# Performance work log

Measured on AMD Instinct MI355X. Metric: run time of the kernel, lower is better.

## Reference

```python
import jax, jax.numpy as jnp
import numpy as np
from jax import lax

E = 20          # num experts / classes
BN_EPS = 1e-5


def _conv(x, w, b=None):
    # NCHW conv, stride 1, 'same' padding (kernel 3x3 or 1x1)
    y = lax.conv_general_dilated(x, w, (1, 1), 'SAME',
                                 dimension_numbers=('NCHW', 'OIHW', 'NCHW'))
    return y if b is None else y + b[None, :, None, None]


def _lrelu(x):
    return jnp.where(x >= 0, x, 0.2 * x)


def _bn(x, g, b, m, v):
    # inference-mode batchnorm
    scale = g * lax.rsqrt(v + BN_EPS)
    return x * scale[None, :, None, None] + (b - m * scale)[None, :, None, None]


def setup_inputs() -> dict:
    key = jax.random.key(0)
    ks = iter(jax.random.split(key, 40))
    def w(shape):
        return jax.random.normal(next(ks), shape, jnp.float32) * 0.05
    d = {}
    d['x'] = jax.random.normal(next(ks), (2, 3, 192, 192), jnp.float32)
    d['noise'] = jax.random.normal(next(ks), (2, 128, 192, 192), jnp.float32)
    # classification head
    d['cls_w1'] = w((64, 3, 3, 3));    d['cls_b1'] = jnp.zeros((64,), jnp.float32)
    d['cls_w2'] = w((128, 64, 3, 3));  d['cls_b2'] = jnp.zeros((128,), jnp.float32)
    d['cls_w3'] = w((256, 128, 3, 3)); d['cls_b3'] = jnp.zeros((256,), jnp.float32)
    d['cls_w4'] = w((512, 256, 1, 1)); d['cls_b4'] = jnp.zeros((512,), jnp.float32)
    d['cls_w5'] = w((E, 512, 1, 1));   d['cls_b5'] = jnp.zeros((E,), jnp.float32)
    for c, i in ((128, 1), (256, 2), (512, 3)):
        d[f'bn{i}_g'] = jnp.ones((c,), jnp.float32)
        d[f'bn{i}_b'] = jnp.zeros((c,), jnp.float32)
        d[f'bn{i}_m'] = jnp.zeros((c,), jnp.float32)
        d[f'bn{i}_v'] = jnp.ones((c,), jnp.float32)
    # 20 expert encoders (stacked on leading axis)
    d['enc_w1'] = w((E, 32, 3, 3, 3));    d['enc_b1'] = jnp.zeros((E, 32), jnp.float32)
    d['enc_w2'] = w((E, 64, 32, 3, 3));   d['enc_b2'] = jnp.zeros((E, 64), jnp.float32)
    d['enc_w3'] = w((E, 128, 64, 3, 3));  d['enc_b3'] = jnp.zeros((E, 128), jnp.float32)
    d['enc_w4'] = w((E, 128, 128, 3, 3)); d['enc_b4'] = jnp.zeros((E, 128), jnp.float32)
    # decoder (legacy=False: first two 1x1 convs have no bias)
    d['dec_w1'] = w((64, 128, 1, 1))
    d['dec_w2'] = w((32, 64, 1, 1))
    d['dec_w3'] = w((3, 32, 1, 1)); d['dec_b3'] = jnp.zeros((3,), jnp.float32)
    return d


def reference(x, noise,
              cls_w1, cls_b1, cls_w2, cls_b2, cls_w3, cls_b3,
              cls_w4, cls_b4, cls_w5, cls_b5,
              bn1_g, bn1_b, bn1_m, bn1_v,
              bn2_g, bn2_b, bn2_m, bn2_v,
              bn3_g, bn3_b, bn3_m, bn3_v,
              enc_w1, enc_b1, enc_w2, enc_b2, enc_w3, enc_b3, enc_w4, enc_b4,
              dec_w1, dec_w2, dec_w3, dec_b3):
    B, _, H, W = x.shape
    C = enc_w4.shape[1]  # 128
    # --- classification / routing ---
    h = _lrelu(_conv(x, cls_w1, cls_b1))
    h = _lrelu(_bn(_conv(h, cls_w2, cls_b2), bn1_g, bn1_b, bn1_m, bn1_v))
    h = _lrelu(_bn(_conv(h, cls_w3, cls_b3), bn2_g, bn2_b, bn2_m, bn2_v))
    h = _lrelu(_bn(_conv(h, cls_w4, cls_b4), bn3_g, bn3_b, bn3_m, bn3_v))
    classes = jax.nn.softmax(_conv(h, cls_w5, cls_b5), axis=1)  # [B,E,H,W]
    idx = jnp.argmax(classes, axis=1)  # [B,H,W] top-1 expert per pixel

    # --- run all 20 dense encoders (faithful to original torch.where masking) ---
    def enc(w1, b1, w2, b2, w3, b3, w4, b4):
        e = _lrelu(_conv(x, w1, b1))
        e = _lrelu(_conv(e, w2, b2))
        e = _lrelu(_conv(e, w3, b3))
        return _conv(e, w4, b4)
    embs = jax.vmap(enc)(enc_w1, enc_b1, enc_w2, enc_b2,
                         enc_w3, enc_b3, enc_w4, enc_b4)  # [E,B,128,H,W]
    embs = jnp.moveaxis(embs, 0, 1)  # [B,E,128,H,W]
    sel_idx = jnp.broadcast_to(idx[:, None, None, :, :], (B, 1, C, H, W))
    emb = jnp.take_along_axis(embs, sel_idx, axis=1)[:, 0]  # [B,128,H,W]

    # --- decode with additive noise ---
    d = _conv(emb + noise, dec_w1)
    d = _conv(d, dec_w2)
    out = _conv(d, dec_w3, dec_b3)  # [B,3,H,W]

    # --- load balancing loss ---
    one_hot = jax.nn.one_hot(idx, E, dtype=jnp.float32)          # [B,H,W,E]
    density = one_hot.reshape(B, -1, E).mean(axis=1)             # [B,E]
    density_proxy = classes.reshape(B, E, -1).mean(axis=-1)      # [B,E]
    lb = (density_proxy * density).mean() * float(E * E)
    return out, lb * 0.1
```

## Files before the change

kernel.cpp:

```cpp
#include <hip/hip_runtime.h>
#include <hip/hip_bf16.h>

typedef __hip_bfloat16 bf16;
typedef unsigned short u16;
typedef short s16x8 __attribute__((ext_vector_type(8)));
typedef float f32x4 __attribute__((ext_vector_type(4)));
#define MFMA16(a, b, c) __builtin_amdgcn_mfma_f32_16x16x32_bf16(a, b, c, 0, 0, 0)

#define HW_   36864
#define WP_   194
#define HWP_  37636
#define W_    192
#define SP_   9216

__device__ __forceinline__ float ldin(const void* p, size_t i, int f32) {
    return f32 ? ((const float*)p)[i] : __bfloat162float(((const bf16*)p)[i]);
}
__device__ __forceinline__ int probe_f32(const void* pr) {
    return ((const unsigned*)pr)[0] == 0x3F800000u;
}
__device__ __forceinline__ u16 f2bf(float f) {
    bf16 h = __float2bfloat16(f);
    return *reinterpret_cast<u16*>(&h);
}

__global__ __launch_bounds__(256) void pad_x_k(const void* __restrict__ x,
                                               float* __restrict__ xpad,
                                               const void* __restrict__ pr) {
    const int f32 = probe_f32(pr);
    int i = blockIdx.x * 256 + threadIdx.x;
    if (i >= 2 * 3 * HW_) return;
    int w = i % W_;
    int h = (i / W_) % W_;
    int c = i / HW_;
    xpad[(size_t)c * HWP_ + (size_t)(h + 1) * WP_ + (w + 1)] = ldin(x, i, f32);
}

__global__ __launch_bounds__(256) void conv3x3_k(
    const float* __restrict__ in, const void* __restrict__ wgt,
    const void* __restrict__ bias, const void* __restrict__ bng,
    const void* __restrict__ bnb, const void* __restrict__ bnm,
    const void* __restrict__ bnv, float* __restrict__ out,
    int Cin, int Cout, int lrelu, const void* __restrict__ pr)
{
    extern __shared__ float wl[];
    const int f32 = probe_f32(pr);
    const int tid = threadIdx.x;
    const int co0 = blockIdx.y * 8;
    const int b   = blockIdx.z;
    const int n = Cin * 72;
    for (int i = tid; i < n; i += 256) {
        int u = i & 7, r = i >> 3;
        int ci = r / 9, tap = r - ci * 9;
        wl[i] = ldin(wgt, ((size_t)(co0 + u) * Cin + ci) * 9 + tap, f32);
    }
    __syncthreads();

    const int pixb = blockIdx.x * 1024 + tid;
    int off[4];
#pragma unroll
    for (int p = 0; p < 4; ++p) {
        int pix = pixb + p * 256;
        int h = pix / W_, w = pix - h * W_;
        off[p] = (h + 1) * WP_ + (w + 1);
    }
    float acc[32];
#pragma unroll
    for (int i = 0; i < 32; ++i) acc[i] = 0.f;

    const int doff[9] = {-(WP_+1), -WP_, -(WP_-1), -1, 0, 1, WP_-1, WP_, WP_+1};
    const float* inb = in + (size_t)b * Cin * HWP_;
    for (int ci = 0; ci < Cin; ++ci) {
        const float* ip = inb + (size_t)ci * HWP_;
        const float* wp = wl + ci * 72;
#pragma unroll
        for (int tap = 0; tap < 9; ++tap) {
            const float4 wa = *(const float4*)(wp + tap * 8);
            const float4 wb = *(const float4*)(wp + tap * 8 + 4);
            const int d = doff[tap];
            float v[4];
#pragma unroll
            for (int p = 0; p < 4; ++p) v[p] = ip[off[p] + d];
#pragma unroll
            for (int p = 0; p < 4; ++p) {
                acc[p*8+0] += v[p] * wa.x;  acc[p*8+1] += v[p] * wa.y;
                acc[p*8+2] += v[p] * wa.z;  acc[p*8+3] += v[p] * wa.w;
                acc[p*8+4] += v[p] * wb.x;  acc[p*8+5] += v[p] * wb.y;
                acc[p*8+6] += v[p] * wb.z;  acc[p*8+7] += v[p] * wb.w;
            }
        }
    }

#pragma unroll
    for (int u = 0; u < 8; ++u) {
        const int co = co0 + u;
        float s = 1.f, t = 0.f;
        if (bng) {
            float g = ldin(bng, co, f32), bb = ldin(bnb, co, f32);
            float m = ldin(bnm, co, f32), vv = ldin(bnv, co, f32);
            s = g * rsqrtf(vv + 1e-5f);
            t = bb - m * s;
        }
        const float bs = bias ? ldin(bias, co, f32) : 0.f;
        float* op = out + ((size_t)b * Cout + co) * HWP_;
#pragma unroll
        for (int p = 0; p < 4; ++p) {
            float val = (acc[p*8+u] + bs) * s + t;
            if (lrelu) val = val >= 0.f ? val : 0.2f * val;
            op[off[p]] = val;
        }
    }
}

__global__ __launch_bounds__(256) void conv1x1s_k(
    const float* __restrict__ in, const void* __restrict__ wgt,
    const void* __restrict__ bias, const void* __restrict__ bng,
    const void* __restrict__ bnb, const void* __restrict__ bnm,
    const void* __restrict__ bnv, float* __restrict__ out,
    int Cin, int pix0, const void* __restrict__ pr)
{
    extern __shared__ float wl[];
    const int f32 = probe_f32(pr);
    const int tid = threadIdx.x;
    const int co0 = blockIdx.y * 8;
    const int b   = blockIdx.z;
    const int n = Cin * 8;
    for (int i = tid; i < n; i += 256) {
        int u = i & 7, ci = i >> 3;
        wl[i] = ldin(wgt, (size_t)(co0 + u) * Cin + ci, f32);
    }
    __syncthreads();

    const int pixb = pix0 + blockIdx.x * 1024 + tid;
    int off[4], lp[4];
#pragma unroll
    for (int p = 0; p < 4; ++p) {
        int pix = pixb + p * 256;
        lp[p] = pix - pix0;
        int h = pix / W_, w = pix - h * W_;
        off[p] = (h + 1) * WP_ + (w + 1);
    }
    float acc[32];
#pragma unroll
    for (int i = 0; i < 32; ++i) acc[i] = 0.f;

    for (int ci = 0; ci < Cin; ++ci) {
        const float* ip = in + ((size_t)b * Cin + ci) * HWP_;
        const float4 wa = *(const float4*)(wl + ci * 8);
        const float4 wb = *(const float4*)(wl + ci * 8 + 4);
        float v[4];
#pragma unroll
        for (int p = 0; p < 4; ++p) v[p] = ip[off[p]];
#pragma unroll
        for (int p = 0; p < 4; ++p) {
            acc[p*8+0] += v[p] * wa.x;  acc[p*8+1] += v[p] * wa.y;
            acc[p*8+2] += v[p] * wa.z;  acc[p*8+3] += v[p] * wa.w;
            acc[p*8+4] += v[p] * wb.x;  acc[p*8+5] += v[p] * wb.y;
            acc[p*8+6] += v[p] * wb.z;  acc[p*8+7] += v[p] * wb.w;
        }
    }

#pragma unroll
    for (int u = 0; u < 8; ++u) {
        const int co = co0 + u;
        float g = ldin(bng, co, f32), bb = ldin(bnb, co, f32);
        float m = ldin(bnm, co, f32), vv = ldin(bnv, co, f32);
        float s = g * rsqrtf(vv + 1e-5f);
        float t = bb - m * s;
        const float bs = ldin(bias, co, f32);
        float* op = out + ((size_t)b * 512 + co) * SP_;
#pragma unroll
        for (int p = 0; p < 4; ++p) {
            float val = (acc[p*8+u] + bs) * s + t;
            val = val >= 0.f ? val : 0.2f * val;
            op[lp[p]] = val;
        }
    }
}

__global__ __launch_bounds__(256) void heads_k(
    const float* __restrict__ c4q, const void* __restrict__ w5,
    const void* __restrict__ b5, int* __restrict__ idx,
    float* __restrict__ proxy, float* __restrict__ cntg, int pix0,
    const void* __restrict__ pr)
{
    extern __shared__ float wl[];
    __shared__ float sums[20];
    __shared__ float cnts[20];
    const int f32 = probe_f32(pr);
    const int tid = threadIdx.x;
    const int b = blockIdx.y;
    for (int i = tid; i < 512 * 20; i += 256) {
        int e = i % 20, ci = i / 20;
        wl[ci * 20 + e] = ldin(w5, (size_t)e * 512 + ci, f32);
    }
    if (tid < 20) { sums[tid] = 0.f; cnts[tid] = 0.f; }
    __syncthreads();

    const int lpix = blockIdx.x * 256 + tid;

    float acc[20];
#pragma unroll
    for (int e = 0; e < 20; ++e) acc[e] = ldin(b5, e, f32);
    const float* ip = c4q + (size_t)b * 512 * SP_;
    for (int ci = 0; ci < 512; ++ci) {
        const float v = ip[(size_t)ci * SP_ + lpix];
        const float* wp = wl + ci * 20;
#pragma unroll
        for (int e = 0; e < 20; ++e) acc[e] += v * wp[e];
    }

    float m = acc[0]; int am = 0;
#pragma unroll
    for (int e = 1; e < 20; ++e) if (acc[e] > m) { m = acc[e]; am = e; }
    float prb[20], ssum = 0.f;
#pragma unroll
    for (int e = 0; e < 20; ++e) { prb[e] = expf(acc[e] - m); ssum += prb[e]; }
    const float inv = 1.f / ssum;
    idx[b * HW_ + pix0 + lpix] = am;

    const int lane = tid & 63;
#pragma unroll
    for (int e = 0; e < 20; ++e) {
        float p = prb[e] * inv;
        p += __shfl_down(p, 32); p += __shfl_down(p, 16); p += __shfl_down(p, 8);
        p += __shfl_down(p, 4);  p += __shfl_down(p, 2);  p += __shfl_down(p, 1);
        if (lane == 0) atomicAdd(&sums[e], p);
        unsigned long long bal = __ballot(am == e);
        if (lane == 0) atomicAdd(&cnts[e], (float)__popcll(bal));
    }
    __syncthreads();
    if (tid < 20) {
        atomicAdd(&proxy[b * 20 + tid], sums[tid]);
        atomicAdd(&cntg[b * 20 + tid], cnts[tid]);
    }
}

__global__ __launch_bounds__(256) void wtx_k(const void* __restrict__ w,
                                             u16* __restrict__ wt,
                                             int Cout, int Cin, int nTot,
                                             const void* __restrict__ pr) {
    const int f32 = probe_f32(pr);
    int i = blockIdx.x * 256 + threadIdx.x;
    if (i >= nTot) return;
    int ci = i % Cin; int r = i / Cin;
    int co = r % Cout; r /= Cout;
    int tap = r % 9; int e = r / 9;
    size_t src = ((size_t)(e * Cout + co) * Cin + ci) * 9 + tap;
    wt[i] = f2bf(ldin(w, src, f32));
}

__global__ __launch_bounds__(512) void fused_expert_k(
    const float* __restrict__ xpad, const int* __restrict__ idx,
    const void* __restrict__ ew1, const void* __restrict__ eb1,
    const u16* __restrict__ Wt2, const void* __restrict__ eb2,
    const u16* __restrict__ Wt3, const void* __restrict__ eb3,
    const u16* __restrict__ Wt4, const void* __restrict__ eb4,
    float* __restrict__ emb, const void* __restrict__ pr)
{
    __shared__ __align__(16) char smem_[137216];
    u16*   e2s = (u16*)smem_;
    u16*   e3s = (u16*)(smem_ + 54272);
    u16*   e1s = (u16*)(smem_ + 54272);
    float* xs  = (float*)smem_;
    float* wl1 = (float*)(smem_ + 6912);
    u16*   w2s = (u16*)(smem_ + 86016);
    __shared__ int s_sel[256];
    __shared__ int s_wc[8];
    __shared__ unsigned long long s_selq[4];
    __shared__ u16 s_l3[324];
    __shared__ int s_c3;

    const int f32 = probe_f32(pr);
    const int tid  = threadIdx.x;
    const int lane = tid & 63, wv = tid >> 6;
    const int ml = lane & 15, q8 = (lane >> 4) * 8, m0 = (lane >> 4) * 4;
    const int b = blockIdx.y;
    const int eid = blockIdx.z;
    const int ty = blockIdx.x / 12, tx = blockIdx.x - ty * 12;
    const int Oh = ty * 16, Ow = tx * 16;

    {
        int sel = 0;
        if (tid < 256) {
            const int r = tid >> 4, c = tid & 15;
            sel = (idx[b * HW_ + (Oh + r) * W_ + (Ow + c)] == eid);
        }
        const unsigned long long m = __ballot(sel);
        if (lane == 0) {
            s_wc[wv] = __popcll(m);
            if (wv < 4) s_selq[wv] = m;
        }
        __syncthreads();
        int cnt = 0;
#pragma unroll
        for (int w = 0; w < 8; ++w) cnt += s_wc[w];
        if (cnt == 0) return;
        int pre = 0;
        for (int w = 0; w < wv; ++w) pre += s_wc[w];
        if (sel)
            s_sel[pre + __popcll(m & ((1ull << lane) - 1ull))] = tid;
    }

    if (wv == 0) {
        unsigned need = 0;
        const int r3 = lane;
        if (r3 < 18) {
            unsigned m = 0;
#pragma unroll
            for (int d = 0; d < 3; ++d) {
                const int r = r3 - 2 + d;
                if (r >= 0 && r < 16)
                    m |= (unsigned)((s_selq[r >> 2] >> ((r & 3) * 16)) & 0xFFFFull);
            }
            need = (m | (m << 1) | (m << 2)) & 0x3FFFFu;
        }
        const int pc = __popc(need);
        int inc = pc;
#pragma unroll
        for (int o = 1; o < 32; o <<= 1) {
            const int t = __shfl_up(inc, o);
            if (lane >= o) inc += t;
        }
        int k = inc - pc;
        unsigned mm = need;
        while (mm) {
            const int c = __ffs(mm) - 1;
            mm &= mm - 1;
            s_l3[k++] = (u16)(r3 * 18 + c);
        }
        if (lane == 17) s_c3 = inc;
    }

    for (int i = tid; i < 24 * 24 * 3; i += 512) {
        int ch = i % 3, pxl = i / 3;
        int r = pxl / 24, c = pxl - r * 24;
        int ir = Oh - 4 + r, ic = Ow - 4 + c;
        float v = 0.f;
        if (ir >= -1 && ir < 193 && ic >= -1 && ic < 193)
            v = xpad[((size_t)b * 3 + ch) * HWP_ + (size_t)(ir + 1) * WP_ + (ic + 1)];
        xs[pxl * 3 + ch] = v;
    }
    for (int i = tid; i < 896; i += 512) {
        if (i < 864) {
            int co = i & 31, k = i >> 5;
            int ci = k / 9, tap = k - ci * 9;
            wl1[i] = ldin(ew1, (size_t)eid * 864 + ((size_t)co * 3 + ci) * 9 + tap, f32);
        } else {
            wl1[i] = ldin(eb1, (size_t)eid * 32 + (i - 864), f32);
        }
    }
    {
        const u16* Wt2e = Wt2 + (size_t)eid * 9 * 64 * 32;
        for (int i = tid; i < 2304; i += 512) {
            int r = i >> 2, part = i & 3;
            *(uint4*)(w2s + (size_t)r * 40 + part * 8) =
                *(const uint4*)(Wt2e + (size_t)r * 32 + part * 8);
        }
    }
    __syncthreads();

    if (tid < 484) {
        const int p = tid;
        const int r1 = p / 22, c1 = p - r1 * 22;
        const int ir = Oh - 3 + r1, ic = Ow - 3 + c1;
        const int inimg = (ir >= 0 && ir < 192 && ic >= 0 && ic < 192);
        float a1[32];
#pragma unroll
        for (int co = 0; co < 32; ++co) a1[co] = 0.f;
        if (inimg) {
#pragma unroll
            for (int ci = 0; ci < 3; ++ci)
#pragma unroll
                for (int tap = 0; tap < 9; ++tap) {
                    const int dy = tap / 3, dx = tap - dy * 3;
                    const float xv = xs[((r1 + dy) * 24 + (c1 + dx)) * 3 + ci];
                    const float* wp = wl1 + (ci * 9 + tap) * 32;
#pragma unroll
                    for (int co = 0; co < 32; ++co) a1[co] += xv * wp[co];
                }
        }
        u16 pk[32];
#pragma unroll
        for (int co = 0; co < 32; ++co) {
            float v = 0.f;
            if (inimg) {
                v = a1[co] + wl1[864 + co];
                v = v >= 0.f ? v : 0.2f * v;
            }
            pk[co] = f2bf(v);
        }
#pragma unroll
        for (int ch = 0; ch < 4; ++ch)
            *(uint4*)(e1s + ((size_t)ch * 488 + p) * 8) = ((const uint4*)pk)[ch];
    }
    __syncthreads();

    {
        int pxv[4], r2v[4], c2v[4];
#pragma unroll
        for (int j = 0; j < 4; ++j) {
            int t = wv + 8 * j; if (t > 24) t = 24;
            int px = t * 16 + ml;
            pxv[j] = px; r2v[j] = px / 20; c2v[j] = px - (px / 20) * 20;
        }
        f32x4 acc2[4][4];
#pragma unroll
        for (int j = 0; j < 4; ++j)
#pragma unroll
            for (int n = 0; n < 4; ++n) acc2[j][n] = (f32x4){0.f,0.f,0.f,0.f};

#pragma unroll
        for (int tap = 0; tap < 9; ++tap) {
            const int dy = tap / 3, dx = tap - dy * 3;
            s16x8 aW[4];
#pragma unroll
            for (int n = 0; n < 4; ++n)
                aW[n] = *(const s16x8*)(w2s + ((size_t)tap * 64 + n * 16 + ml) * 40 + q8);
#pragma unroll
            for (int j = 0; j < 4; ++j) {
                const int lin = (r2v[j] + dy) * 22 + (c2v[j] + dx);
                const s16x8 bA = *(const s16x8*)(e1s + ((size_t)(q8 >> 3) * 488 + lin) * 8);
#pragma unroll
                for (int n = 0; n < 4; ++n) acc2[j][n] = MFMA16(aW[n], bA, acc2[j][n]);
            }
        }
        __syncthreads();
#pragma unroll
        for (int j = 0; j < 4; ++j) {
            const int px = pxv[j];
            const int r2 = r2v[j], c2 = c2v[j];
            const int ir = Oh - 2 + r2, ic = Ow - 2 + c2;
            const int inimg = (ir >= 0 && ir < 192 && ic >= 0 && ic < 192);
#pragma unroll
            for (int n = 0; n < 4; ++n) {
                u16 pk[4];
#pragma unroll
                for (int r = 0; r < 4; ++r) {
                    const int co = n * 16 + m0 + r;
                    float v = 0.f;
                    if (inimg) {
                        v = acc2[j][n][r] + ldin(eb2, (size_t)eid * 64 + co, f32);
                        v = v >= 0.f ? v : 0.2f * v;
                    }
                    pk[r] = f2bf(v);
                }
                const int chunk = (n * 16 + m0) >> 3;
                *(uint2*)(e2s + ((size_t)chunk * 424 + px) * 8 + (m0 & 4)) = *(const uint2*)pk;
            }
        }
    }
    __syncthreads();

    {
        const u16* Wt3e = Wt3 + (size_t)eid * 9 * 128 * 64;
        const int np = wv >> 2;
        const int w4 = wv & 3;
        const int cnt3 = s_c3;
        const int tiles3 = (cnt3 + 15) >> 4;
        const int jc = (w4 < tiles3) ? ((tiles3 - w4 + 3) >> 2) : 0;
        int pxv[6], r3v[6], c3v[6];
#pragma unroll
        for (int j = 0; j < 6; ++j) {
            int li = (w4 + 4 * j) * 16 + ml;
            if (li >= cnt3) li = cnt3 - 1;
            const int px = s_l3[li];
            pxv[j] = px; r3v[j] = px / 18; c3v[j] = px - (px / 18) * 18;
        }
        f32x4 acc3[6][4];
#pragma unroll
        for (int j = 0; j < 6; ++j)
#pragma unroll
            for (int n = 0; n < 4; ++n) acc3[j][n] = (f32x4){0.f,0.f,0.f,0.f};

#define LW3(dst, g) { const int tp_ = (g) >> 1, cc_ = (g) & 1;                         \
    dst[0] = *(const s16x8*)(Wt3e + ((size_t)tp_*128 + np*64 +  0 + ml)*64 + cc_*32 + q8); \
    dst[1] = *(const s16x8*)(Wt3e + ((size_t)tp_*128 + np*64 + 16 + ml)*64 + cc_*32 + q8); \
    dst[2] = *(const s16x8*)(Wt3e + ((size_t)tp_*128 + np*64 + 32 + ml)*64 + cc_*32 + q8); \
    dst[3] = *(const s16x8*)(Wt3e + ((size_t)tp_*128 + np*64 + 48 + ml)*64 + cc_*32 + q8); }
#define C3GROUP(BUF, g) { const int tp_ = (g) >> 1, cc_ = (g) & 1;                     \
    const int dy_ = tp_ / 3, dx_ = tp_ - dy_ * 3;                                      \
    const int ch_ = cc_ * 4 + (q8 >> 3);                                               \
    _Pragma("unroll")                                                                  \
    for (int j = 0; j < 6; ++j) if (j < jc) {                                          \
        const int lin_ = (r3v[j] + dy_) * 20 + (c3v[j] + dx_);                         \
        const s16x8 bA_ = *(const s16x8*)(e2s + ((size_t)ch_ * 424 + lin_) * 8);       \
        acc3[j][0] = MFMA16(BUF[0], bA_, acc3[j][0]);                                  \
        acc3[j][1] = MFMA16(BUF[1], bA_, acc3[j][1]);                                  \
        acc3[j][2] = MFMA16(BUF[2], bA_, acc3[j][2]);                                  \
        acc3[j][3] = MFMA16(BUF[3], bA_, acc3[j][3]); } }

        s16x8 aA[4], aB[4];
        LW3(aA, 0);
#pragma unroll
        for (int g = 0; g < 18; g += 2) {
            LW3(aB, g + 1);
            C3GROUP(aA, g);
            if (g + 2 < 18) LW3(aA, g + 2);
            C3GROUP(aB, g + 1);
        }
#undef LW3
#undef C3GROUP

        float b3[4][4];
#pragma unroll
        for (int n = 0; n < 4; ++n)
#pragma unroll
            for (int r = 0; r < 4; ++r)
                b3[n][r] = ldin(eb3, (size_t)eid * 128 + np * 64 + n * 16 + m0 + r, f32);
#pragma unroll
        for (int j = 0; j < 6; ++j) {
            if (j >= jc) continue;
            const int px = pxv[j];
            const int r3 = r3v[j], c3 = c3v[j];
            const int ir = Oh - 1 + r3, ic = Ow - 1 + c3;
            const int inimg = (ir >= 0 && ir < 192 && ic >= 0 && ic < 192);
#pragma unroll
            for (int n = 0; n < 4; ++n) {
                u16 pk[4];
#pragma unroll
                for (int r = 0; r < 4; ++r) {
                    float v = 0.f;
                    if (inimg) {
                        v = acc3[j][n][r] + b3[n][r];
                        v = v >= 0.f ? v : 0.2f * v;
                    }
                    pk[r] = f2bf(v);
                }
                const int chunk = (np * 64 + n * 16 + m0) >> 3;
                *(uint2*)(e3s + ((size_t)chunk * 324 + px) * 8 + (m0 & 4)) = *(const uint2*)pk;
            }
        }
    }
    __syncthreads();

    {
        const u16* Wt4e = Wt4 + (size_t)eid * 9 * 128 * 128;
        int cnt = 0;
#pragma unroll
        for (int w = 0; w < 8; ++w) cnt += s_wc[w];
        const int mtiles = (cnt + 15) >> 4;
        const int n0 = wv * 16;
        float bs[4];
#pragma unroll
        for (int r = 0; r < 4; ++r) bs[r] = ldin(eb4, (size_t)eid * 128 + n0 + m0 + r, f32);

#define LW4(dst, g) { const int tp_ = (g) >> 2, c0_ = ((g) & 3) * 32;                  \
    dst = *(const s16x8*)(Wt4e + ((size_t)tp_ * 128 + n0 + ml) * 128 + c0_ + q8); }
#define C4GROUP(BUF, g) { const int tp_ = (g) >> 2, cq_ = ((g) & 3) * 32 + q8;         \
    const int dy_ = tp_ / 3, dx_ = tp_ - dy_ * 3;                                      \
    const size_t cb_ = (size_t)(cq_ >> 3) * 324;                                       \
    _Pragma("unroll")                                                                  \
    for (int u = 0; u < 4; ++u) if (u < mc) {                                          \
        const int lin_ = (rrv[u] + dy_) * 18 + (ccv[u] + dx_);                         \
        const s16x8 bA_ = *(const s16x8*)(e3s + (cb_ + lin_) * 8);                     \
        acc4[u] = MFMA16(BUF, bA_, acc4[u]); } }

        for (int mt0 = 0; mt0 < mtiles; mt0 += 4) {
            const int mc = (mtiles - mt0 < 4) ? (mtiles - mt0) : 4;
            int rrv[4], ccv[4], liv[4];
#pragma unroll
            for (int u = 0; u < 4; ++u) {
                const int li = (mt0 + u) * 16 + ml;
                int lc = li; if (lc >= cnt) lc = cnt - 1;
                const int lpx = s_sel[lc];
                liv[u] = li; rrv[u] = lpx >> 4; ccv[u] = lpx & 15;
            }
            f32x4 acc4[4];
#pragma unroll
            for (int u = 0; u < 4; ++u) acc4[u] = (f32x4){0.f,0.f,0.f,0.f};

            s16x8 wA, wB, wC, wD;
            LW4(wA, 0); LW4(wB, 1);
#pragma unroll
            for (int g = 0; g < 36; g += 4) {
                LW4(wC, g + 2);
                LW4(wD, g + 3);
                C4GROUP(wA, g);
                C4GROUP(wB, g + 1);
                if (g + 4 < 36) LW4(wA, g + 4);
                if (g + 5 < 36) LW4(wB, g + 5);
                C4GROUP(wC, g + 2);
                C4GROUP(wD, g + 3);
            }
#pragma unroll
            for (int u = 0; u < 4; ++u) {
                if (u < mc && liv[u] < cnt) {
                    const int g2 = (Oh + rrv[u]) * W_ + Ow + ccv[u];
#pragma unroll
                    for (int r = 0; r < 4; ++r)
                        emb[((size_t)b * 128 + n0 + m0 + r) * HW_ + g2] = acc4[u][r] + bs[r];
                }
            }
        }
#undef LW4
#undef C4GROUP
    }
}

__global__ __launch_bounds__(256) void dec_fused_k(
    const float* __restrict__ emb, const void* __restrict__ noise,
    const void* __restrict__ dw1, const void* __restrict__ dw2,
    const void* __restrict__ dw3, const void* __restrict__ db3,
    void* __restrict__ outb, const void* __restrict__ pr)
{
    __shared__ float w1s[128 * 64];
    __shared__ float w2s[64 * 32];
    __shared__ float w3s[100];
    const int f32 = probe_f32(pr);
    const int tid = threadIdx.x;
    for (int i = tid; i < 128 * 64; i += 256) {
        int ci = i >> 6, co = i & 63;
        w1s[i] = ldin(dw1, (size_t)co * 128 + ci, f32);
    }
    for (int i = tid; i < 64 * 32; i += 256) {
        int ci = i >> 5, co = i & 31;
        w2s[i] = ldin(dw2, (size_t)co * 64 + ci, f32);
    }
    if (tid < 96) {
        int ci = tid / 3, k = tid - ci * 3;
        w3s[ci * 3 + k] = ldin(dw3, (size_t)k * 32 + ci, f32);
    }
    if (tid >= 96 && tid < 99) w3s[96 + tid - 96] = ldin(db3, tid - 96, f32);
    __syncthreads();

    const int b = blockIdx.y;
    const int pix = blockIdx.x * 256 + tid;

    float h1[64];
#pragma unroll
    for (int i = 0; i < 64; ++i) h1[i] = 0.f;
    for (int ci = 0; ci < 128; ++ci) {
        const size_t base = ((size_t)b * 128 + ci) * HW_ + pix;
        const float v = emb[base] + ldin(noise, base, f32);
        const float* wp = w1s + ci * 64;
#pragma unroll
        for (int c4 = 0; c4 < 16; ++c4) {
            const float4 w = *(const float4*)(wp + c4 * 4);
            h1[c4*4+0] += v * w.x; h1[c4*4+1] += v * w.y;
            h1[c4*4+2] += v * w.z; h1[c4*4+3] += v * w.w;
        }
    }
    float h2[32];
#pragma unroll
    for (int i = 0; i < 32; ++i) h2[i] = 0.f;
#pragma unroll
    for (int ci = 0; ci < 64; ++ci) {
        const float v = h1[ci];
        const float* wp = w2s + ci * 32;
#pragma unroll
        for (int c4 = 0; c4 < 8; ++c4) {
            const float4 w = *(const float4*)(wp + c4 * 4);
            h2[c4*4+0] += v * w.x; h2[c4*4+1] += v * w.y;
            h2[c4*4+2] += v * w.z; h2[c4*4+3] += v * w.w;
        }
    }
    float a0 = w3s[96], a1 = w3s[97], a2 = w3s[98];
#pragma unroll
    for (int ci = 0; ci < 32; ++ci) {
        const float v = h2[ci];
        a0 += v * w3s[ci * 3 + 0];
        a1 += v * w3s[ci * 3 + 1];
        a2 += v * w3s[ci * 3 + 2];
    }
    const size_t o0 = (size_t)(b * 3 + 0) * HW_ + pix;
    const size_t o1 = (size_t)(b * 3 + 1) * HW_ + pix;
    const size_t o2 = (size_t)(b * 3 + 2) * HW_ + pix;
    if (f32) {
        ((float*)outb)[o0] = a0; ((float*)outb)[o1] = a1; ((float*)outb)[o2] = a2;
    } else {
        ((bf16*)outb)[o0] = __float2bfloat16(a0);
        ((bf16*)outb)[o1] = __float2bfloat16(a1);
        ((bf16*)outb)[o2] = __float2bfloat16(a2);
    }
}

__global__ void lb_k(const float* __restrict__ proxy, const float* __restrict__ cnt,
                     void* __restrict__ out, const void* __restrict__ pr) {
    const int f32 = probe_f32(pr);
    const int t = threadIdx.x;
    const float inv = 1.0f / (float)HW_;
    float v = 0.f;
    if (t < 40) v = (proxy[t] * inv) * (cnt[t] * inv);
#pragma unroll
    for (int o = 32; o > 0; o >>= 1) v += __shfl_down(v, o);
    if (t == 0) {
        if (f32) ((float*)out)[221184] = v;
        else     ((bf16*)out)[221184] = __float2bfloat16(v);
    }
}

extern "C" void kernel_launch(void* const* d_in, const int* in_sizes, int n_in,
                              void* d_out, int out_size, void* d_ws, size_t ws_size,
                              hipStream_t stream) {
    (void)in_sizes; (void)n_in; (void)out_size; (void)ws_size;
    const void* x    = d_in[0];
    const void* noise= d_in[1];
    const void* cw1  = d_in[2];  const void* cb1 = d_in[3];
    const void* cw2  = d_in[4];  const void* cb2 = d_in[5];
    const void* cw3  = d_in[6];  const void* cb3 = d_in[7];
    const void* cw4  = d_in[8];  const void* cb4 = d_in[9];
    const void* cw5  = d_in[10]; const void* cb5 = d_in[11];
    const void* bn1g = d_in[12]; const void* bn1b = d_in[13];
    const void* bn1m = d_in[14]; const void* bn1v = d_in[15];
    const void* bn2g = d_in[16]; const void* bn2b = d_in[17];
    const void* bn2m = d_in[18]; const void* bn2v = d_in[19];
    const void* bn3g = d_in[20]; const void* bn3b = d_in[21];
    const void* bn3m = d_in[22]; const void* bn3v = d_in[23];
    const void* ew1  = d_in[24]; const void* eb1 = d_in[25];
    const void* ew2  = d_in[26]; const void* eb2 = d_in[27];
    const void* ew3  = d_in[28]; const void* eb3 = d_in[29];
    const void* ew4  = d_in[30]; const void* eb4 = d_in[31];
    const void* dw1  = d_in[32];
    const void* dw2  = d_in[33];
    const void* dw3  = d_in[34]; const void* db3 = d_in[35];
    const void* pr   = bn1v;

    char* ws = (char*)d_ws;
    constexpr size_t SZ_XPAD = (((size_t)2*3*HWP_*4) + 255) & ~(size_t)255;
    constexpr size_t O_BUF2  = SZ_XPAD;
    constexpr size_t SZ_BUF2 = (size_t)2*256*HWP_*4;
    constexpr size_t O_BUF1  = O_BUF2 + SZ_BUF2;
    constexpr size_t SZ_BUF1 = (size_t)2*128*HWP_*4;
    constexpr size_t O_IDX   = O_BUF1 + SZ_BUF1;
    constexpr size_t O_STAT  = O_IDX + (size_t)2*HW_*4;
    constexpr size_t WS_USED = O_STAT + 512;

    float* xpad  = (float*)(ws);
    float* buf2  = (float*)(ws + O_BUF2);
    int*   idx   = (int*)  (ws + O_IDX);
    float* proxy = (float*)(ws + O_STAT);
    float* cntg  = proxy + 40;

    float* c1  = buf2;
    float* c3  = buf2;
    float* c2  = (float*)(ws + O_BUF1);
    float* c4q = (float*)(ws + O_BUF1);
    float* emb = buf2;
    u16* Wt2 = (u16*)(ws + O_BUF1);
    u16* Wt3 = Wt2 + 368640;
    u16* Wt4 = Wt3 + 1474560;

    hipMemsetAsync(d_ws, 0, WS_USED, stream);

    dim3 blk(256);
    pad_x_k<<<dim3((2*3*HW_ + 255)/256), blk, 0, stream>>>(x, xpad, pr);

    conv3x3_k<<<dim3(36,  8, 2), blk,   3*288, stream>>>(xpad, cw1, cb1, nullptr,nullptr,nullptr,nullptr, c1,   3,  64, 1, pr);
    conv3x3_k<<<dim3(36, 16, 2), blk,  64*288, stream>>>(c1,   cw2, cb2, bn1g,bn1b,bn1m,bn1v,           c2,  64, 128, 1, pr);
    conv3x3_k<<<dim3(36, 32, 2), blk, 128*288, stream>>>(c2,   cw3, cb3, bn2g,bn2b,bn2m,bn2v,           c3, 128, 256, 1, pr);
    for (int s = 0; s < 4; ++s) {
        conv1x1s_k<<<dim3(9, 64, 2), blk, 256*32, stream>>>(c3, cw4, cb4, bn3g,bn3b,bn3m,bn3v, c4q, 256, s*SP_, pr);
        heads_k<<<dim3(36, 2), blk, 512*20*4, stream>>>(c4q, cw5, cb5, idx, proxy, cntg, s*SP_, pr);
    }

    wtx_k<<<dim3(1440),  blk, 0, stream>>>(ew2, Wt2,  64,  32,  368640, pr);
    wtx_k<<<dim3(5760),  blk, 0, stream>>>(ew3, Wt3, 128,  64, 1474560, pr);
    wtx_k<<<dim3(11520), blk, 0, stream>>>(ew4, Wt4, 128, 128, 2949120, pr);

    fused_expert_k<<<dim3(144, 2, 20), dim3(512), 0, stream>>>(
        xpad, idx, ew1, eb1, Wt2, eb2, Wt3, eb3, Wt4, eb4, emb, pr);

    dec_fused_k<<<dim3(144, 2), blk, 0, stream>>>(emb, noise, dw1, dw2, dw3, db3, d_out, pr);
    lb_k<<<1, 64, 0, stream>>>(proxy, cntg, d_out, pr);
}
```

Before: 2.508 ms.

## Build compact tile-expert worklist and run expert kernel as persistent work queue

The heads kernel now records, per 16x16 tile, a bitmask of which experts are selected, and a small kernel compacts these masks into a list of (tile, expert) work items. The fused expert kernel becomes a persistent grid of 256 blocks that pull items from an atomic counter, double-buffering the next item index in shared memory, instead of launching 5760 blocks that mostly exit early. Bias loads for layer 2 are also hoisted into registers. The aim is to remove launch and early-exit scheduling overhead for empty tile-expert pairs and to balance load, at the cost of extra atomics and a serial loop per block.

```diff
diff --git a/kernel.cpp b/kernel.cpp
--- a/kernel.cpp
+++ b/kernel.cpp
@@ -181,7 +181,8 @@
 __global__ __launch_bounds__(256) void heads_k(
     const float* __restrict__ c4q, const void* __restrict__ w5,
     const void* __restrict__ b5, int* __restrict__ idx,
-    float* __restrict__ proxy, float* __restrict__ cntg, int pix0,
+    float* __restrict__ proxy, float* __restrict__ cntg,
+    unsigned* __restrict__ expmask, int pix0,
     const void* __restrict__ pr)
 {
     extern __shared__ float wl[];
@@ -218,6 +219,11 @@
     for (int e = 0; e < 20; ++e) { prb[e] = expf(acc[e] - m); ssum += prb[e]; }
     const float inv = 1.f / ssum;
     idx[b * HW_ + pix0 + lpix] = am;
+    {
+        const int pg = pix0 + lpix;
+        const int ph = pg / W_, pw = pg - ph * W_;
+        atomicOr(&expmask[b * 288 + (ph >> 4) * 12 + (pw >> 4)], 1u << am);
+    }
 
     const int lane = tid & 63;
 #pragma unroll
@@ -233,6 +239,20 @@
     if (tid < 20) {
         atomicAdd(&proxy[b * 20 + tid], sums[tid]);
         atomicAdd(&cntg[b * 20 + tid], cnts[tid]);
+    }
+}
+
+__global__ __launch_bounds__(192) void wlb_k(const unsigned* __restrict__ expmask,
+                                             unsigned* __restrict__ wklist,
+                                             int* __restrict__ wkcnt) {
+    const int t = blockIdx.x * 192 + threadIdx.x;
+    if (t >= 576) return;
+    unsigned m = expmask[t];
+    while (m) {
+        const int e = __ffs(m) - 1;
+        m &= m - 1;
+        const int k = atomicAdd(wkcnt, 1);
+        wklist[k] = ((unsigned)t << 5) | (unsigned)e;
     }
 }
 
@@ -256,7 +276,9 @@
     const u16* __restrict__ Wt2, const void* __restrict__ eb2,
     const u16* __restrict__ Wt3, const void* __restrict__ eb3,
     const u16* __restrict__ Wt4, const void* __restrict__ eb4,
-    float* __restrict__ emb, const void* __restrict__ pr)
+    float* __restrict__ emb,
+    const unsigned* __restrict__ wklist, int* __restrict__ wkctr,
+    const int* __restrict__ wkcnt, const void* __restrict__ pr)
 {
     __shared__ __align__(16) char smem_[137216];
     u16*   e2s = (u16*)smem_;
@@ -270,208 +292,228 @@
     __shared__ unsigned long long s_selq[4];
     __shared__ u16 s_l3[324];
     __shared__ int s_c3;
+    __shared__ int s_it[2];
 
     const int f32 = probe_f32(pr);
     const int tid  = threadIdx.x;
     const int lane = tid & 63, wv = tid >> 6;
     const int ml = lane & 15, q8 = (lane >> 4) * 8, m0 = (lane >> 4) * 4;
-    const int b = blockIdx.y;
-    const int eid = blockIdx.z;
-    const int ty = blockIdx.x / 12, tx = blockIdx.x - ty * 12;
-    const int Oh = ty * 16, Ow = tx * 16;
-
-    {
-        int sel = 0;
-        if (tid < 256) {
-            const int r = tid >> 4, c = tid & 15;
-            sel = (idx[b * HW_ + (Oh + r) * W_ + (Ow + c)] == eid);
-        }
-        const unsigned long long m = __ballot(sel);
-        if (lane == 0) {
-            s_wc[wv] = __popcll(m);
-            if (wv < 4) s_selq[wv] = m;
-        }
+
+    const int tot = *wkcnt;
+    if (tid == 0) s_it[0] = atomicAdd(wkctr, 1);
+
+    for (int p = 0; ; p ^= 1) {
         __syncthreads();
-        int cnt = 0;
-#pragma unroll
-        for (int w = 0; w < 8; ++w) cnt += s_wc[w];
-        if (cnt == 0) return;
-        int pre = 0;
-        for (int w = 0; w < wv; ++w) pre += s_wc[w];
-        if (sel)
-            s_sel[pre + __popcll(m & ((1ull << lane) - 1ull))] = tid;
-    }
-
-    if (wv == 0) {
-        unsigned need = 0;
-        const int r3 = lane;
-        if (r3 < 18) {
-            unsigned m = 0;
-#pragma unroll
-            for (int d = 0; d < 3; ++d) {
-                const int r = r3 - 2 + d;
-                if (r >= 0 && r < 16)
-                    m |= (unsigned)((s_selq[r >> 2] >> ((r & 3) * 16)) & 0xFFFFull);
-            }
-            need = (m | (m << 1) | (m << 2)) & 0x3FFFFu;
-        }
-        const int pc = __popc(need);
-        int inc = pc;
-#pragma unroll
-        for (int o = 1; o < 32; o <<= 1) {
-            const int t = __shfl_up(inc, o);
-            if (lane >= o) inc += t;
-        }
-        int k = inc - pc;
-        unsigned mm = need;
-        while (mm) {
-            const int c = __ffs(mm) - 1;
-            mm &= mm - 1;
-            s_l3[k++] = (u16)(r3 * 18 + c);
-        }
-        if (lane == 17) s_c3 = inc;
-    }
-
-    for (int i = tid; i < 24 * 24 * 3; i += 512) {
-        int ch = i % 3, pxl = i / 3;
-        int r = pxl / 24, c = pxl - r * 24;
-        int ir = Oh - 4 + r, ic = Ow - 4 + c;
-        float v = 0.f;
-        if (ir >= -1 && ir < 193 && ic >= -1 && ic < 193)
-            v = xpad[((size_t)b * 3 + ch) * HWP_ + (size_t)(ir + 1) * WP_ + (ic + 1)];
-        xs[pxl * 3 + ch] = v;
-    }
-    for (int i = tid; i < 896; i += 512) {
-        if (i < 864) {
-            int co = i & 31, k = i >> 5;
-            int ci = k / 9, tap = k - ci * 9;
-            wl1[i] = ldin(ew1, (size_t)eid * 864 + ((size_t)co * 3 + ci) * 9 + tap, f32);
-        } else {
-            wl1[i] = ldin(eb1, (size_t)eid * 32 + (i - 864), f32);
-        }
-    }
-    {
-        const u16* Wt2e = Wt2 + (size_t)eid * 9 * 64 * 32;
-        for (int i = tid; i < 2304; i += 512) {
-            int r = i >> 2, part = i & 3;
-            *(uint4*)(w2s + (size_t)r * 40 + part * 8) =
-                *(const uint4*)(Wt2e + (size_t)r * 32 + part * 8);
-        }
-    }
-    __syncthreads();
-
-    if (tid < 484) {
-        const int p = tid;
-        const int r1 = p / 22, c1 = p - r1 * 22;
-        const int ir = Oh - 3 + r1, ic = Ow - 3 + c1;
-        const int inimg = (ir >= 0 && ir < 192 && ic >= 0 && ic < 192);
-        float a1[32];
-#pragma unroll
-        for (int co = 0; co < 32; ++co) a1[co] = 0.f;
-        if (inimg) {
-#pragma unroll
-            for (int ci = 0; ci < 3; ++ci)
-#pragma unroll
-                for (int tap = 0; tap < 9; ++tap) {
-                    const int dy = tap / 3, dx = tap - dy * 3;
-                    const float xv = xs[((r1 + dy) * 24 + (c1 + dx)) * 3 + ci];
-                    const float* wp = wl1 + (ci * 9 + tap) * 32;
-#pragma unroll
-                    for (int co = 0; co < 32; ++co) a1[co] += xv * wp[co];
+        const int item = s_it[p];
+        if (item >= tot) return;
+        if (tid == 0) s_it[p ^ 1] = atomicAdd(wkctr, 1);
+
+        const unsigned wk = wklist[item];
+        const int eid = wk & 31;
+        const int tlin = wk >> 5;
+        const int b = tlin / 288;
+        const int tl = tlin - b * 288;
+        const int ty = tl / 12, tx = tl - ty * 12;
+        const int Oh = ty * 16, Ow = tx * 16;
+
+        int cnt;
+        {
+            int sel = 0;
+            if (tid < 256) {
+                const int r = tid >> 4, c = tid & 15;
+                sel = (idx[b * HW_ + (Oh + r) * W_ + (Ow + c)] == eid);
+            }
+            const unsigned long long m = __ballot(sel);
+            if (lane == 0) {
+                s_wc[wv] = __popcll(m);
+                if (wv < 4) s_selq[wv] = m;
+            }
+            __syncthreads();
+            cnt = 0;
+#pragma unroll
+            for (int w = 0; w < 8; ++w) cnt += s_wc[w];
+            int pre = 0;
+            for (int w = 0; w < wv; ++w) pre += s_wc[w];
+            if (sel)
+                s_sel[pre + __popcll(m & ((1ull << lane) - 1ull))] = tid;
+        }
+        if (cnt == 0) continue;
+
+        if (wv == 0) {
+            unsigned need = 0;
+            const int r3 = lane;
+            if (r3 < 18) {
+                unsigned m = 0;
+#pragma unroll
+                for (int d = 0; d < 3; ++d) {
+                    const int r = r3 - 2 + d;
+                    if (r >= 0 && r < 16)
+                        m |= (unsigned)((s_selq[r >> 2] >> ((r & 3) * 16)) & 0xFFFFull);
                 }
-        }
-        u16 pk[32];
-#pragma unroll
-        for (int co = 0; co < 32; ++co) {
+                need = (m | (m << 1) | (m << 2)) & 0x3FFFFu;
+            }
+            const int pc = __popc(need);
+            int inc = pc;
+#pragma unroll
+            for (int o = 1; o < 32; o <<= 1) {
+                const int t = __shfl_up(inc, o);
+                if (lane >= o) inc += t;
+            }
+            int k = inc - pc;
+            unsigned mm = need;
+            while (mm) {
+                const int c = __ffs(mm) - 1;
+                mm &= mm - 1;
+                s_l3[k++] = (u16)(r3 * 18 + c);
+            }
+            if (lane == 17) s_c3 = inc;
+        }
+
+        for (int i = tid; i < 24 * 24 * 3; i += 512) {
+            int ch = i % 3, pxl = i / 3;
+            int r = pxl / 24, c = pxl - r * 24;
+            int ir = Oh - 4 + r, ic = Ow - 4 + c;
             float v = 0.f;
+            if (ir >= -1 && ir < 193 && ic >= -1 && ic < 193)
+                v = xpad[((size_t)b * 3 + ch) * HWP_ + (size_t)(ir + 1) * WP_ + (ic + 1)];
+            xs[pxl * 3 + ch] = v;
+        }
+        for (int i = tid; i < 896; i += 512) {
+            if (i < 864) {
+                int co = i & 31, k = i >> 5;
+                int ci = k / 9, tap = k - ci * 9;
+                wl1[i] = ldin(ew1, (size_t)eid * 864 + ((size_t)co * 3 + ci) * 9 + tap, f32);
+            } else {
+                wl1[i] = ldin(eb1, (size_t)eid * 32 + (i - 864), f32);
+            }
+        }
+        {
+            const u16* Wt2e = Wt2 + (size_t)eid * 9 * 64 * 32;
+            for (int i = tid; i < 2304; i += 512) {
+                int r = i >> 2, part = i & 3;
+                *(uint4*)(w2s + (size_t)r * 40 + part * 8) =
+                    *(const uint4*)(Wt2e + (size_t)r * 32 + part * 8);
+            }
+        }
+        __syncthreads();
+
+        if (tid < 484) {
+            const int pp = tid;
+            const int r1 = pp / 22, c1 = pp - r1 * 22;
+            const int ir = Oh - 3 + r1, ic = Ow - 3 + c1;
+            const int inimg = (ir >= 0 && ir < 192 && ic >= 0 && ic < 192);
+            float a1[32];
+#pragma unroll
+            for (int co = 0; co < 32; ++co) a1[co] = 0.f;
             if (inimg) {
-                v = a1[co] + wl1[864 + co];
-                v = v >= 0.f ? v : 0.2f * v;
-            }
-            pk[co] = f2bf(v);
-        }
-#pragma unroll
-        for (int ch = 0; ch < 4; ++ch)
-            *(uint4*)(e1s + ((size_t)ch * 488 + p) * 8) = ((const uint4*)pk)[ch];
-    }
-    __syncthreads();
-
-    {
-        int pxv[4], r2v[4], c2v[4];
-#pragma unroll
-        for (int j = 0; j < 4; ++j) {
-            int t = wv + 8 * j; if (t > 24) t = 24;
-            int px = t * 16 + ml;
-            pxv[j] = px; r2v[j] = px / 20; c2v[j] = px - (px / 20) * 20;
-        }
-        f32x4 acc2[4][4];
-#pragma unroll
-        for (int j = 0; j < 4; ++j)
-#pragma unroll
-            for (int n = 0; n < 4; ++n) acc2[j][n] = (f32x4){0.f,0.f,0.f,0.f};
-
-#pragma unroll
-        for (int tap = 0; tap < 9; ++tap) {
-            const int dy = tap / 3, dx = tap - dy * 3;
-            s16x8 aW[4];
+#pragma unroll
+                for (int ci = 0; ci < 3; ++ci)
+#pragma unroll
+                    for (int tap = 0; tap < 9; ++tap) {
+                        const int dy = tap / 3, dx = tap - dy * 3;
+                        const float xv = xs[((r1 + dy) * 24 + (c1 + dx)) * 3 + ci];
+                        const float* wp = wl1 + (ci * 9 + tap) * 32;
+#pragma unroll
+                        for (int co = 0; co < 32; ++co) a1[co] += xv * wp[co];
+                    }
+            }
+            u16 pk[32];
+#pragma unroll
+            for (int co = 0; co < 32; ++co) {
+                float v = 0.f;
+                if (inimg) {
+                    v = a1[co] + wl1[864 + co];
+                    v = v >= 0.f ? v : 0.2f * v;
+                }
+                pk[co] = f2bf(v);
+            }
+#pragma unroll
+            for (int ch = 0; ch < 4; ++ch)
+                *(uint4*)(e1s + ((size_t)ch * 488 + pp) * 8) = ((const uint4*)pk)[ch];
+        }
+        __syncthreads();
+
+        {
+            int pxv[4], r2v[4], c2v[4];
+#pragma unroll
+            for (int j = 0; j < 4; ++j) {
+                int t = wv + 8 * j; if (t > 24) t = 24;
+                int px = t * 16 + ml;
+                pxv[j] = px; r2v[j] = px / 20; c2v[j] = px - (px / 20) * 20;
+            }
+            f32x4 acc2[4][4];
+#pragma unroll
+            for (int j = 0; j < 4; ++j)
+#pragma unroll
+                for (int n = 0; n < 4; ++n) acc2[j][n] = (f32x4){0.f,0.f,0.f,0.f};
+
+#pragma unroll
+            for (int tap = 0; tap < 9; ++tap) {
+                const int dy = tap / 3, dx = tap - dy * 3;
+                s16x8 aW[4];
+#pragma unroll
+                for (int n = 0; n < 4; ++n)
+                    aW[n] = *(const s16x8*)(w2s + ((size_t)tap * 64 + n * 16 + ml) * 40 + q8);
+#pragma unroll
+                for (int j = 0; j < 4; ++j) {
+                    const int lin = (r2v[j] + dy) * 22 + (c2v[j] + dx);
+                    const s16x8 bA = *(const s16x8*)(e1s + ((size_t)(q8 >> 3) * 488 + lin) * 8);
+#pragma unroll
+                    for (int n = 0; n < 4; ++n) acc2[j][n] = MFMA16(aW[n], bA, acc2[j][n]);
+                }
+            }
+            __syncthreads();
+            float b2r[4][4];
 #pragma unroll
             for (int n = 0; n < 4; ++n)
-                aW[n] = *(const s16x8*)(w2s + ((size_t)tap * 64 + n * 16 + ml) * 40 + q8);
+#pragma unroll
+                for (int r = 0; r < 4; ++r)
+                    b2r[n][r] = ldin(eb2, (size_t)eid * 64 + n * 16 + m0 + r, f32);
 #pragma unroll
             for (int j = 0; j < 4; ++j) {
-                const int lin = (r2v[j] + dy) * 22 + (c2v[j] + dx);
-                const s16x8 bA = *(const s16x8*)(e1s + ((size_t)(q8 >> 3) * 488 + lin) * 8);
-#pragma unroll
-                for (int n = 0; n < 4; ++n) acc2[j][n] = MFMA16(aW[n], bA, acc2[j][n]);
+                const int px = pxv[j];
+                const int r2 = r2v[j], c2 = c2v[j];
+                const int ir = Oh - 2 + r2, ic = Ow - 2 + c2;
+                const int inimg = (ir >= 0 && ir < 192 && ic >= 0 && ic < 192);
+#pragma unroll
+                for (int n = 0; n < 4; ++n) {
+                    u16 pk[4];
+#pragma unroll
+                    for (int r = 0; r < 4; ++r) {
+                        float v = 0.f;
+                        if (inimg) {
+                            v = acc2[j][n][r] + b2r[n][r];
+                            v = v >= 0.f ? v : 0.2f * v;
+                        }
+                        pk[r] = f2bf(v);
+                    }
+                    const int chunk = (n * 16 + m0) >> 3;
+                    *(uint2*)(e2s + ((size_t)chunk * 424 + px) * 8 + (m0 & 4)) = *(const uint2*)pk;
+                }
             }
         }
         __syncthreads();
-#pragma unroll
-        for (int j = 0; j < 4; ++j) {
-            const int px = pxv[j];
-            const int r2 = r2v[j], c2 = c2v[j];
-            const int ir = Oh - 2 + r2, ic = Ow - 2 + c2;
-            const int inimg = (ir >= 0 && ir < 192 && ic >= 0 && ic < 192);
-#pragma unroll
-            for (int n = 0; n < 4; ++n) {
-                u16 pk[4];
-#pragma unroll
-                for (int r = 0; r < 4; ++r) {
-                    const int co = n * 16 + m0 + r;
-                    float v = 0.f;
-                    if (inimg) {
-                        v = acc2[j][n][r] + ldin(eb2, (size_t)eid * 64 + co, f32);
-                        v = v >= 0.f ? v : 0.2f * v;
-                    }
-                    pk[r] = f2bf(v);
-                }
-                const int chunk = (n * 16 + m0) >> 3;
-                *(uint2*)(e2s + ((size_t)chunk * 424 + px) * 8 + (m0 & 4)) = *(const uint2*)pk;
-            }
-        }
-    }
-    __syncthreads();
-
-    {
-        const u16* Wt3e = Wt3 + (size_t)eid * 9 * 128 * 64;
-        const int np = wv >> 2;
-        const int w4 = wv & 3;
-        const int cnt3 = s_c3;
-        const int tiles3 = (cnt3 + 15) >> 4;
-        const int jc = (w4 < tiles3) ? ((tiles3 - w4 + 3) >> 2) : 0;
-        int pxv[6], r3v[6], c3v[6];
-#pragma unroll
-        for (int j = 0; j < 6; ++j) {
-            int li = (w4 + 4 * j) * 16 + ml;
-            if (li >= cnt3) li = cnt3 - 1;
-            const int px = s_l3[li];
-            pxv[j] = px; r3v[j] = px / 18; c3v[j] = px - (px / 18) * 18;
-        }
-        f32x4 acc3[6][4];
-#pragma unroll
-        for (int j = 0; j < 6; ++j)
-#pragma unroll
-            for (int n = 0; n < 4; ++n) acc3[j][n] = (f32x4){0.f,0.f,0.f,0.f};
+
+        {
+            const u16* Wt3e = Wt3 + (size_t)eid * 9 * 128 * 64;
+            const int np = wv >> 2;
+            const int w4 = wv & 3;
+            const int cnt3 = s_c3;
+            const int tiles3 = (cnt3 + 15) >> 4;
+            const int jc = (w4 < tiles3) ? ((tiles3 - w4 + 3) >> 2) : 0;
+            int pxv[6], r3v[6], c3v[6];
+#pragma unroll
+            for (int j = 0; j < 6; ++j) {
+                int li = (w4 + 4 * j) * 16 + ml;
+                if (li >= cnt3) li = cnt3 - 1;
+                const int px = s_l3[li];
+                pxv[j] = px; r3v[j] = px / 18; c3v[j] = px - (px / 18) * 18;
+            }
+            f32x4 acc3[6][4];
+#pragma unroll
+            for (int j = 0; j < 6; ++j)
+#pragma unroll
+                for (int n = 0; n < 4; ++n) acc3[j][n] = (f32x4){0.f,0.f,0.f,0.f};
 
 #define LW3(dst, g) { const int tp_ = (g) >> 1, cc_ = (g) & 1;                         \
     dst[0] = *(const s16x8*)(Wt3e + ((size_t)tp_*128 + np*64 +  0 + ml)*64 + cc_*32 + q8); \
@@ -490,60 +532,57 @@
         acc3[j][2] = MFMA16(BUF[2], bA_, acc3[j][2]);                                  \
         acc3[j][3] = MFMA16(BUF[3], bA_, acc3[j][3]); } }
 
-        s16x8 aA[4], aB[4];
-        LW3(aA, 0);
-#pragma unroll
-        for (int g = 0; g < 18; g += 2) {
-            LW3(aB, g + 1);
-            C3GROUP(aA, g);
-            if (g + 2 < 18) LW3(aA, g + 2);
-            C3GROUP(aB, g + 1);
-        }
+            s16x8 aA[4], aB[4];
+            LW3(aA, 0);
+#pragma unroll
+            for (int g = 0; g < 18; g += 2) {
+                LW3(aB, g + 1);
+                C3GROUP(aA, g);
+                if (g + 2 < 18) LW3(aA, g + 2);
+                C3GROUP(aB, g + 1);
+            }
 #undef LW3
 #undef C3GROUP
 
-        float b3[4][4];
-#pragma unroll
-        for (int n = 0; n < 4; ++n)
-#pragma unroll
-            for (int r = 0; r < 4; ++r)
-                b3[n][r] = ldin(eb3, (size_t)eid * 128 + np * 64 + n * 16 + m0 + r, f32);
-#pragma unroll
-        for (int j = 0; j < 6; ++j) {
-            if (j >= jc) continue;
-            const int px = pxv[j];
-            const int r3 = r3v[j], c3 = c3v[j];
-            const int ir = Oh - 1 + r3, ic = Ow - 1 + c3;
-            const int inimg = (ir >= 0 && ir < 192 && ic >= 0 && ic < 192);
-#pragma unroll
-            for (int n = 0; n < 4; ++n) {
-                u16 pk[4];
-#pragma unroll
-                for (int r = 0; r < 4; ++r) {
-                    float v = 0.f;
-                    if (inimg) {
-                        v = acc3[j][n][r] + b3[n][r];
-                        v = v >= 0.f ? v : 0.2f * v;
+            float b3[4][4];
+#pragma unroll
+            for (int n = 0; n < 4; ++n)
+#pragma unroll
+                for (int r = 0; r < 4; ++r)
+                    b3[n][r] = ldin(eb3, (size_t)eid * 128 + np * 64 + n * 16 + m0 + r, f32);
+#pragma unroll
+            for (int j = 0; j < 6; ++j) {
+                if (j >= jc) continue;
+                const int px = pxv[j];
+                const int r3 = r3v[j], c3 = c3v[j];
+                const int ir = Oh - 1 + r3, ic = Ow - 1 + c3;
+                const int inimg = (ir >= 0 && ir < 192 && ic >= 0 && ic < 192);
+#pragma unroll
+                for (int n = 0; n < 4; ++n) {
+                    u16 pk[4];
+#pragma unroll
+                    for (int r = 0; r < 4; ++r) {
+                        float v = 0.f;
+                        if (inimg) {
+                            v = acc3[j][n][r] + b3[n][r];
+                            v = v >= 0.f ? v : 0.2f * v;
+                        }
+                        pk[r] = f2bf(v);
                     }
-                    pk[r] = f2bf(v);
+                    const int chunk = (np * 64 + n * 16 + m0) >> 3;
+                    *(uint2*)(e3s + ((size_t)chunk * 324 + px) * 8 + (m0 & 4)) = *(const uint2*)pk;
                 }
-                const int chunk = (np * 64 + n * 16 + m0) >> 3;
-                *(uint2*)(e3s + ((size_t)chunk * 324 + px) * 8 + (m0 & 4)) = *(const uint2*)pk;
-            }
-        }
-    }
-    __syncthreads();
-
-    {
-        const u16* Wt4e = Wt4 + (size_t)eid * 9 * 128 * 128;
-        int cnt = 0;
-#pragma unroll
-        for (int w = 0; w < 8; ++w) cnt += s_wc[w];
-        const int mtiles = (cnt + 15) >> 4;
-        const int n0 = wv * 16;
-        float bs[4];
-#pragma unroll
-        for (int r = 0; r < 4; ++r) bs[r] = ldin(eb4, (size_t)eid * 128 + n0 + m0 + r, f32);
+            }
+        }
+        __syncthreads();
+
+        {
+            const u16* Wt4e = Wt4 + (size_t)eid * 9 * 128 * 128;
+            const int mtiles = (cnt + 15) >> 4;
+            const int n0 = wv * 16;
+            float bs[4];
+#pragma unroll
+            for (int r = 0; r < 4; ++r) bs[r] = ldin(eb4, (size_t)eid * 128 + n0 + m0 + r, f32);
 
 #define LW4(dst, g) { const int tp_ = (g) >> 2, c0_ = ((g) & 3) * 32;                  \
     dst = *(const s16x8*)(Wt4e + ((size_t)tp_ * 128 + n0 + ml) * 128 + c0_ + q8); }
@@ -556,45 +595,46 @@
         const s16x8 bA_ = *(const s16x8*)(e3s + (cb_ + lin_) * 8);                     \
         acc4[u] = MFMA16(BUF, bA_, acc4[u]); } }
 
-        for (int mt0 = 0; mt0 < mtiles; mt0 += 4) {
-            const int mc = (mtiles - mt0 < 4) ? (mtiles - mt0) : 4;
-            int rrv[4], ccv[4], liv[4];
-#pragma unroll
-            for (int u = 0; u < 4; ++u) {
-                const int li = (mt0 + u) * 16 + ml;
-                int lc = li; if (lc >= cnt) lc = cnt - 1;
-                const int lpx = s_sel[lc];
-                liv[u] = li; rrv[u] = lpx >> 4; ccv[u] = lpx & 15;
-            }
-            f32x4 acc4[4];
-#pragma unroll
-            for (int u = 0; u < 4; ++u) acc4[u] = (f32x4){0.f,0.f,0.f,0.f};
-
-            s16x8 wA, wB, wC, wD;
-            LW4(wA, 0); LW4(wB, 1);
-#pragma unroll
-            for (int g = 0; g < 36; g += 4) {
-                LW4(wC, g + 2);
-                LW4(wD, g + 3);
-                C4GROUP(wA, g);
-                C4GROUP(wB, g + 1);
-                if (g + 4 < 36) LW4(wA, g + 4);
-                if (g + 5 < 36) LW4(wB, g + 5);
-                C4GROUP(wC, g + 2);
-                C4GROUP(wD, g + 3);
-            }
-#pragma unroll
-            for (int u = 0; u < 4; ++u) {
-                if (u < mc && liv[u] < cnt) {
-                    const int g2 = (Oh + rrv[u]) * W_ + Ow + ccv[u];
-#pragma unroll
-                    for (int r = 0; r < 4; ++r)
-                        emb[((size_t)b * 128 + n0 + m0 + r) * HW_ + g2] = acc4[u][r] + bs[r];
+            for (int mt0 = 0; mt0 < mtiles; mt0 += 4) {
+                const int mc = (mtiles - mt0 < 4) ? (mtiles - mt0) : 4;
+                int rrv[4], ccv[4], liv[4];
+#pragma unroll
+                for (int u = 0; u < 4; ++u) {
+                    const int li = (mt0 + u) * 16 + ml;
+                    int lc = li; if (lc >= cnt) lc = cnt - 1;
+                    const int lpx = s_sel[lc];
+                    liv[u] = li; rrv[u] = lpx >> 4; ccv[u] = lpx & 15;
                 }
-            }
-        }
+                f32x4 acc4[4];
+#pragma unroll
+                for (int u = 0; u < 4; ++u) acc4[u] = (f32x4){0.f,0.f,0.f,0.f};
+
+                s16x8 wA, wB, wC, wD;
+                LW4(wA, 0); LW4(wB, 1);
+#pragma unroll
+                for (int g = 0; g < 36; g += 4) {
+                    LW4(wC, g + 2);
+                    LW4(wD, g + 3);
+                    C4GROUP(wA, g);
+                    C4GROUP(wB, g + 1);
+                    if (g + 4 < 36) LW4(wA, g + 4);
+                    if (g + 5 < 36) LW4(wB, g + 5);
+                    C4GROUP(wC, g + 2);
+                    C4GROUP(wD, g + 3);
+                }
+#pragma unroll
+                for (int u = 0; u < 4; ++u) {
+                    if (u < mc && liv[u] < cnt) {
+                        const int g2 = (Oh + rrv[u]) * W_ + Ow + ccv[u];
+#pragma unroll
+                        for (int r = 0; r < 4; ++r)
+                            emb[((size_t)b * 128 + n0 + m0 + r) * HW_ + g2] = acc4[u][r] + bs[r];
+                    }
+                }
+            }
 #undef LW4
 #undef C4GROUP
+        }
     }
 }
 
@@ -724,13 +764,18 @@
     constexpr size_t SZ_BUF1 = (size_t)2*128*HWP_*4;
     constexpr size_t O_IDX   = O_BUF1 + SZ_BUF1;
     constexpr size_t O_STAT  = O_IDX + (size_t)2*HW_*4;
-    constexpr size_t WS_USED = O_STAT + 512;
+    constexpr size_t O_WL    = O_STAT + 512;
+    constexpr size_t WS_USED = O_WL + 2304 + 23040 + 256;
 
     float* xpad  = (float*)(ws);
     float* buf2  = (float*)(ws + O_BUF2);
     int*   idx   = (int*)  (ws + O_IDX);
     float* proxy = (float*)(ws + O_STAT);
     float* cntg  = proxy + 40;
+    unsigned* expmask = (unsigned*)(ws + O_WL);
+    unsigned* wklist  = expmask + 576;
+    int*      wkctr   = (int*)(wklist + 5760);
+    int*      wkcnt   = wkctr + 1;
 
     float* c1  = buf2;
     float* c3  = buf2;
@@ -751,15 +796,18 @@
     conv3x3_k<<<dim3(36, 32, 2), blk, 128*288, stream>>>(c2,   cw3, cb3, bn2g,bn2b,bn2m,bn2v,           c3, 128, 256, 1, pr);
     for (int s = 0; s < 4; ++s) {
         conv1x1s_k<<<dim3(9, 64, 2), blk, 256*32, stream>>>(c3, cw4, cb4, bn3g,bn3b,bn3m,bn3v, c4q, 256, s*SP_, pr);
-        heads_k<<<dim3(36, 2), blk, 512*20*4, stream>>>(c4q, cw5, cb5, idx, proxy, cntg, s*SP_, pr);
-    }
+        heads_k<<<dim3(36, 2), blk, 512*20*4, stream>>>(c4q, cw5, cb5, idx, proxy, cntg, expmask, s*SP_, pr);
+    }
+
+    wlb_k<<<dim3(3), dim3(192), 0, stream>>>(expmask, wklist, wkcnt);
 
     wtx_k<<<dim3(1440),  blk, 0, stream>>>(ew2, Wt2,  64,  32,  368640, pr);
     wtx_k<<<dim3(5760),  blk, 0, stream>>>(ew3, Wt3, 128,  64, 1474560, pr);
     wtx_k<<<dim3(11520), blk, 0, stream>>>(ew4, Wt4, 128, 128, 2949120, pr);
 
-    fused_expert_k<<<dim3(144, 2, 20), dim3(512), 0, stream>>>(
-        xpad, idx, ew1, eb1, Wt2, eb2, Wt3, eb3, Wt4, eb4, emb, pr);
+    fused_expert_k<<<dim3(256), dim3(512), 0, stream>>>(
+        xpad, idx, ew1, eb1, Wt2, eb2, Wt3, eb3, Wt4, eb4, emb,
+        wklist, wkctr, wkcnt, pr);
 
     dec_fused_k<<<dim3(144, 2), blk, 0, stream>>>(emb, noise, dw1, dw2, dw3, db3, d_out, pr);
     lb_k<<<1, 64, 0, stream>>>(proxy, cntg, d_out, pr);
```

New measurement: 2.729 ms. 8.8% more time.
